# Performance work log

Measured on AMD Instinct MI355X. Metric: run time of the kernel, lower is better.

## Reference

```python
import jax, jax.numpy as jnp
import numpy as np

B, Q, S, D, H = 8, 100, 4096, 256, 8
HD = D // H
EPS = 1e-5


def layer_norm(x, g, b):
    mu = jnp.mean(x, axis=-1, keepdims=True)
    var = jnp.mean(jnp.square(x - mu), axis=-1, keepdims=True)
    return (x - mu) * jax.lax.rsqrt(var + EPS) * g + b


def mha(q_in, k_in, v_in, w_in, b_in, w_out, b_out, bias=None):
    # torch nn.MultiheadAttention math (batch_first, dropout=0)
    wq, wk, wv = jnp.split(w_in, 3, axis=0)
    bq, bk, bv = jnp.split(b_in, 3, axis=0)
    Bq, Lq, _ = q_in.shape
    Lk = k_in.shape[1]
    q = (q_in @ wq.T + bq).reshape(Bq, Lq, H, HD)
    k = (k_in @ wk.T + bk).reshape(Bq, Lk, H, HD)
    v = (v_in @ wv.T + bv).reshape(Bq, Lk, H, HD)
    scores = jnp.einsum('bqhd,bkhd->bhqk', q, k) / jnp.sqrt(jnp.asarray(HD, q.dtype))
    if bias is not None:
        scores = scores + bias  # [B,1,Q,S] broadcast over heads (same per head)
    attn = jax.nn.softmax(scores, axis=-1)
    out = jnp.einsum('bhqk,bkhd->bqhd', attn, v).reshape(Bq, Lq, D)
    return out @ w_out.T + b_out


def setup_inputs() -> dict:
    key = jax.random.key(0)
    ks = jax.random.split(key, 12)
    s = 0.02
    return {
        'queries': jax.random.normal(ks[0], (B, Q, D), jnp.float32),
        'pixel_feat': jax.random.normal(ks[1], (B, S, D), jnp.float32),
        'prev_mask': jax.random.normal(ks[2], (B, Q, S), jnp.float32),
        'cross_in_w': jax.random.normal(ks[3], (3 * D, D), jnp.float32) * s,
        'cross_in_b': jnp.zeros((3 * D,), jnp.float32),
        'cross_out_w': jax.random.normal(ks[4], (D, D), jnp.float32) * s,
        'cross_out_b': jnp.zeros((D,), jnp.float32),
        'self_in_w': jax.random.normal(ks[5], (3 * D, D), jnp.float32) * s,
        'self_in_b': jnp.zeros((3 * D,), jnp.float32),
        'self_out_w': jax.random.normal(ks[6], (D, D), jnp.float32) * s,
        'self_out_b': jnp.zeros((D,), jnp.float32),
        'ln_cross_g': jnp.ones((D,), jnp.float32),
        'ln_cross_b': jnp.zeros((D,), jnp.float32),
        'ln_self_g': jnp.ones((D,), jnp.float32),
        'ln_self_b': jnp.zeros((D,), jnp.float32),
        'ln_ffn_g': jnp.ones((D,), jnp.float32),
        'ln_ffn_b': jnp.zeros((D,), jnp.float32),
        'ffn_w1': jax.random.normal(ks[7], (4 * D, D), jnp.float32) * s,
        'ffn_b1': jnp.zeros((4 * D,), jnp.float32),
        'ffn_w2': jax.random.normal(ks[8], (D, 4 * D), jnp.float32) * s,
        'ffn_b2': jnp.zeros((D,), jnp.float32),
    }


def reference(queries, pixel_feat, prev_mask,
              cross_in_w, cross_in_b, cross_out_w, cross_out_b,
              self_in_w, self_in_b, self_out_w, self_out_b,
              ln_cross_g, ln_cross_b, ln_self_g, ln_self_b, ln_ffn_g, ln_ffn_b,
              ffn_w1, ffn_b1, ffn_w2, ffn_b2):
    # masked cross-attn bias (no-grad region in torch; boolean ops have no grad)
    region = jax.nn.sigmoid(prev_mask) > 0.5                    # [B,Q,S]
    any_pos = jnp.any(region, axis=-1, keepdims=True)
    region = jnp.where(any_pos, region, jnp.ones_like(region))
    bias = (~region).astype(queries.dtype) * -10000.0
    bias = bias[:, None, :, :]                                  # [B,1,Q,S]

    q_out = mha(layer_norm(queries, ln_cross_g, ln_cross_b), pixel_feat, pixel_feat,
                cross_in_w, cross_in_b, cross_out_w, cross_out_b, bias)
    queries = queries + q_out

    q_norm = layer_norm(queries, ln_self_g, ln_self_b)
    q_out = mha(q_norm, q_norm, q_norm, self_in_w, self_in_b, self_out_w, self_out_b)
    queries = queries + q_out

    h = layer_norm(queries, ln_ffn_g, ln_ffn_b)
    h = jax.nn.gelu(h @ ffn_w1.T + ffn_b1, approximate=False) @ ffn_w2.T + ffn_b2
    return queries + h
```

## Files before the change

kernel.cpp:

```cpp
#include <hip/hip_runtime.h>
#include <hip/hip_bf16.h>
#include <math.h>

#define BQ 100
#define SB 8
#define SS 4096
#define DD 256
#define HH 8
#define HDD 32
#define NSPLIT 4
#define SCHUNK (SS / NSPLIT)
#define MROWS 800

typedef __attribute__((ext_vector_type(8))) short bf16x8;
typedef __attribute__((ext_vector_type(4))) float f32x4;

__device__ inline unsigned short f2bf(float f) {
    union { float f; unsigned u; } v; v.f = f;
    unsigned r = v.u + 0x7fff + ((v.u >> 16) & 1);
    return (unsigned short)(r >> 16);
}

__device__ inline unsigned pkbf(float x, float y) {
    union { __hip_bfloat162 h; unsigned u; } c;
    c.h = __float22bfloat162_rn(make_float2(x, y));
    return c.u;
}

__device__ inline bf16x8 load_bf8(const float* p) {
    float4 a = *(const float4*)p;
    float4 b = *(const float4*)(p + 4);
    union { unsigned u[4]; bf16x8 v; } r;
    r.u[0] = pkbf(a.x, a.y); r.u[1] = pkbf(a.z, a.w);
    r.u[2] = pkbf(b.x, b.y); r.u[3] = pkbf(b.z, b.w);
    return r.v;
}

#define TM 128
#define TN 128
#define TK 32
#define LSTR 40

__global__ __launch_bounds__(256, 4) void stage1(
        const float* __restrict__ queries,
        const float* __restrict__ ln_g, const float* __restrict__ ln_b,
        const float* __restrict__ cw, const float* __restrict__ cb,
        float* __restrict__ q_cross,
        const float* __restrict__ pixel_feat,
        unsigned short* __restrict__ Kb, unsigned short* __restrict__ Vb,
        const float* __restrict__ mask, unsigned* __restrict__ Mbits) {
    __shared__ __align__(16) char smem[21504];
    const int bid = blockIdx.x;
    const int t = threadIdx.x;

    if (bid < 1024) {
        typedef unsigned short (*tile_t)[LSTR];
        tile_t As = (tile_t)smem;
        tile_t Bs = (tile_t)(smem + 128 * LSTR * 2);
        const float* A = pixel_feat;
        const float* W = cw + (size_t)DD * DD;
        const float* bias = cb + DD;
        int xcd = bid & 7, idx = bid >> 3;
        int mt = xcd + 8 * (idx >> 2);
        int nt = idx & 3;
        int m0 = mt * TM, n0 = nt * TN;
        int wave = t / 64, lane = t % 64;
        int wm = (wave % 2) * 64, wn = (wave / 2) * 64;
        int lr = t / 4, lc = (t % 4) * 8;
        int fr = lane % 16, quad = lane / 16;
        f32x4 acc[4][4] = {};
        for (int k0 = 0; k0 < DD; k0 += TK) {
            __syncthreads();
#pragma unroll
            for (int half = 0; half < 2; half++) {
                int r = lr + half * 64;
                float4 a0 = *(const float4*)(A + (size_t)(m0 + r) * DD + k0 + lc);
                float4 a1 = *(const float4*)(A + (size_t)(m0 + r) * DD + k0 + lc + 4);
                uint4 pa;
                pa.x = pkbf(a0.x, a0.y); pa.y = pkbf(a0.z, a0.w);
                pa.z = pkbf(a1.x, a1.y); pa.w = pkbf(a1.z, a1.w);
                *(uint4*)&As[r][lc] = pa;
                float4 b0 = *(const float4*)(W + (size_t)(n0 + r) * DD + k0 + lc);
                float4 b1 = *(const float4*)(W + (size_t)(n0 + r) * DD + k0 + lc + 4);
                uint4 pb;
                pb.x = pkbf(b0.x, b0.y); pb.y = pkbf(b0.z, b0.w);
                pb.z = pkbf(b1.x, b1.y); pb.w = pkbf(b1.z, b1.w);
                *(uint4*)&Bs[r][lc] = pb;
            }
            __syncthreads();
            bf16x8 af[4], bf[4];
#pragma unroll
            for (int mi = 0; mi < 4; mi++)
                af[mi] = *(const bf16x8*)&As[wm + mi * 16 + fr][quad * 8];
#pragma unroll
            for (int ni = 0; ni < 4; ni++)
                bf[ni] = *(const bf16x8*)&Bs[wn + ni * 16 + fr][quad * 8];
#pragma unroll
            for (int mi = 0; mi < 4; mi++)
#pragma unroll
                for (int ni = 0; ni < 4; ni++)
                    acc[mi][ni] = __builtin_amdgcn_mfma_f32_16x16x32_bf16(
                        af[mi], bf[ni], acc[mi][ni], 0, 0, 0);
        }
#pragma unroll
        for (int ni = 0; ni < 4; ni++) {
            int n = n0 + wn + ni * 16 + fr;
            float bv = bias[n];
            unsigned short* dst = (n < 256) ? Kb : Vb;
            int hh = (n >> 5) & 7, d = n & 31;
#pragma unroll
            for (int mi = 0; mi < 4; mi++) {
#pragma unroll
                for (int r = 0; r < 4; r++) {
                    int m = m0 + wm + mi * 16 + quad * 4 + r;
                    int bb = m >> 12, s = m & (SS - 1);
                    dst[((((size_t)bb * HH + hh) * SS + s) << 5) + d] =
                        f2bf(acc[mi][ni][r] + bv);
                }
            }
        }
    } else if (bid < 1824) {
        int row = bid - 1024;
        unsigned* words = (unsigned*)smem;
        unsigned* orred = (unsigned*)(smem + 512);
        int w = t >> 6, lane = t & 63;
        unsigned lor = 0;
        for (int i = 0; i < 16; i++) {
            int s = (w * 16 + i) * 64 + lane;
            unsigned long long bal = __ballot(mask[(size_t)row * SS + s] > 0.f);
            if (lane == 0) {
                words[(w * 16 + i) * 2] = (unsigned)bal;
                words[(w * 16 + i) * 2 + 1] = (unsigned)(bal >> 32);
            }
            lor |= (unsigned)(bal | (bal >> 32));
        }
        if (lane == 0) orred[w] = lor;
        __syncthreads();
        unsigned anyv = orred[0] | orred[1] | orred[2] | orred[3];
        if (t < 128) Mbits[(size_t)row * 128 + t] = anyv ? words[t] : 0xFFFFFFFFu;
    } else {
        typedef unsigned short (*arow_t)[264];
        arow_t Aq = (arow_t)smem;
        float* mu_s = (float*)(smem + 16896);
        float* rs_s = mu_s + 32;
        float (*prt)[8][2] = (float(*)[8][2])(rs_s + 32);
        int idx = bid - 1824;
        int nq = idx & 1, my = idx >> 1;
        int m0 = my * 32;
        int row = t & 31, cs = t >> 5;
        const float* xp = queries + (size_t)(m0 + row) * DD + cs * 32;
        float s = 0.f, ss = 0.f;
#pragma unroll
        for (int c = 0; c < 32; c += 4) {
            float4 v = *(const float4*)(xp + c);
            s += v.x + v.y + v.z + v.w;
            ss += v.x * v.x + v.y * v.y + v.z * v.z + v.w * v.w;
        }
        prt[row][cs][0] = s; prt[row][cs][1] = ss;
        __syncthreads();
        if (t < 32) {
            float sum = 0.f, sq = 0.f;
#pragma unroll
            for (int k = 0; k < 8; k++) { sum += prt[t][k][0]; sq += prt[t][k][1]; }
            float mu = sum * (1.0f / DD);
            float var = sq * (1.0f / DD) - mu * mu;
            mu_s[t] = mu;
            rs_s[t] = rsqrtf(var + 1e-5f);
        }
        __syncthreads();
        {
            float mu = mu_s[row], r = rs_s[row];
            int col0 = cs * 32;
#pragma unroll
            for (int c = 0; c < 32; c += 8) {
                int col = col0 + c;
                float4 v0 = *(const float4*)(xp + c);
                float4 v1 = *(const float4*)(xp + c + 4);
                float4 g0 = *(const float4*)(ln_g + col);
                float4 g1 = *(const float4*)(ln_g + col + 4);
                float4 b0 = *(const float4*)(ln_b + col);
                float4 b1 = *(const float4*)(ln_b + col + 4);
                uint4 pk;
                pk.x = pkbf((v0.x - mu) * r * g0.x + b0.x, (v0.y - mu) * r * g0.y + b0.y);
                pk.y = pkbf((v0.z - mu) * r * g0.z + b0.z, (v0.w - mu) * r * g0.w + b0.w);
                pk.z = pkbf((v1.x - mu) * r * g1.x + b1.x, (v1.y - mu) * r * g1.y + b1.y);
                pk.w = pkbf((v1.z - mu) * r * g1.z + b1.z, (v1.w - mu) * r * g1.w + b1.w);
                *(uint4*)&Aq[row][col] = pk;
            }
        }
        __syncthreads();
        int w = t >> 6, lane = t & 63;
        int fr = lane & 15, quad = lane >> 4;
        int n0 = nq * 128 + w * 32;
        f32x4 acc[2][2] = {};
        const float* Wp0 = cw + (size_t)(n0 + fr) * DD + quad * 8;
        const float* Wp1 = Wp0 + (size_t)16 * DD;
#pragma unroll
        for (int k0 = 0; k0 < DD; k0 += 32) {
            bf16x8 a0 = *(const bf16x8*)&Aq[fr][k0 + quad * 8];
            bf16x8 a1 = *(const bf16x8*)&Aq[16 + fr][k0 + quad * 8];
            bf16x8 w0 = load_bf8(Wp0 + k0);
            bf16x8 w1 = load_bf8(Wp1 + k0);
            acc[0][0] = __builtin_amdgcn_mfma_f32_16x16x32_bf16(a0, w0, acc[0][0], 0, 0, 0);
            acc[0][1] = __builtin_amdgcn_mfma_f32_16x16x32_bf16(a0, w1, acc[0][1], 0, 0, 0);
            acc[1][0] = __builtin_amdgcn_mfma_f32_16x16x32_bf16(a1, w0, acc[1][0], 0, 0, 0);
            acc[1][1] = __builtin_amdgcn_mfma_f32_16x16x32_bf16(a1, w1, acc[1][1], 0, 0, 0);
        }
#pragma unroll
        for (int ni = 0; ni < 2; ni++) {
            int n = n0 + ni * 16 + fr;
            float bv = cb[n];
#pragma unroll
            for (int mi = 0; mi < 2; mi++) {
#pragma unroll
                for (int r = 0; r < 4; r++) {
                    int m = m0 + mi * 16 + quad * 4 + r;
                    q_cross[(size_t)m * DD + n] = acc[mi][ni][r] + bv;
                }
            }
        }
    }
}

template<int MODE>
__global__ __launch_bounds__(64, 4) void ln_gemm(
        const float* __restrict__ X, const float* __restrict__ gam,
        const float* __restrict__ bet,
        const float* __restrict__ W, const float* __restrict__ bias,
        const float* __restrict__ res,
        float* __restrict__ C, int N) {
    __shared__ unsigned short As[32][264];
    __shared__ float mu_s[32], rs_s[32];
    __shared__ float prt[32][2][2];
    const int t = threadIdx.x;
    const int fr = t & 15, quad = t >> 4;
    const int m0 = blockIdx.y * 32, n0 = blockIdx.x * 32;
    const int row = t & 31, half = t >> 5;

    const float* xp = X + (size_t)(m0 + row) * DD + half * 128;
    float s = 0.f, ss = 0.f;
#pragma unroll
    for (int c = 0; c < 128; c += 4) {
        float4 v = *(const float4*)(xp + c);
        s += v.x + v.y + v.z + v.w;
        ss += v.x * v.x + v.y * v.y + v.z * v.z + v.w * v.w;
    }
    prt[row][half][0] = s;
    prt[row][half][1] = ss;
    __syncthreads();
    if (t < 32) {
        float sum = prt[t][0][0] + prt[t][1][0];
        float sq  = prt[t][0][1] + prt[t][1][1];
        float mu = sum * (1.0f / DD);
        float var = sq * (1.0f / DD) - mu * mu;
        mu_s[t] = mu;
        rs_s[t] = rsqrtf(var + 1e-5f);
    }
    __syncthreads();
    {
        float mu = mu_s[row], r = rs_s[row];
#pragma unroll
        for (int c = 0; c < 128; c += 8) {
            int col = half * 128 + c;
            float4 v0 = *(const float4*)(xp + c);
            float4 v1 = *(const float4*)(xp + c + 4);
            float4 g0 = *(const float4*)(gam + col);
            float4 g1 = *(const float4*)(gam + col + 4);
            float4 b0 = *(const float4*)(bet + col);
            float4 b1 = *(const float4*)(bet + col + 4);
            uint4 pk;
            pk.x = pkbf((v0.x - mu) * r * g0.x + b0.x, (v0.y - mu) * r * g0.y + b0.y);
            pk.y = pkbf((v0.z - mu) * r * g0.z + b0.z, (v0.w - mu) * r * g0.w + b0.w);
            pk.z = pkbf((v1.x - mu) * r * g1.x + b1.x, (v1.y - mu) * r * g1.y + b1.y);
            pk.w = pkbf((v1.z - mu) * r * g1.z + b1.z, (v1.w - mu) * r * g1.w + b1.w);
            *(uint4*)&As[row][col] = pk;
        }
    }
    __syncthreads();

    f32x4 acc[2][2] = {};
    const float* Wp0 = W + (size_t)(n0 + fr) * DD + quad * 8;
    const float* Wp1 = Wp0 + (size_t)16 * DD;
#pragma unroll
    for (int k0 = 0; k0 < DD; k0 += 32) {
        bf16x8 a0 = *(const bf16x8*)&As[fr][k0 + quad * 8];
        bf16x8 a1 = *(const bf16x8*)&As[16 + fr][k0 + quad * 8];
        bf16x8 w0 = load_bf8(Wp0 + k0);
        bf16x8 w1 = load_bf8(Wp1 + k0);
        acc[0][0] = __builtin_amdgcn_mfma_f32_16x16x32_bf16(a0, w0, acc[0][0], 0, 0, 0);
        acc[0][1] = __builtin_amdgcn_mfma_f32_16x16x32_bf16(a0, w1, acc[0][1], 0, 0, 0);
        acc[1][0] = __builtin_amdgcn_mfma_f32_16x16x32_bf16(a1, w0, acc[1][0], 0, 0, 0);
        acc[1][1] = __builtin_amdgcn_mfma_f32_16x16x32_bf16(a1, w1, acc[1][1], 0, 0, 0);
    }

#pragma unroll
    for (int ni = 0; ni < 2; ni++) {
        int n = n0 + ni * 16 + fr;
        float bv = bias[n];
#pragma unroll
        for (int mi = 0; mi < 2; mi++) {
#pragma unroll
            for (int r = 0; r < 4; r++) {
                int m = m0 + mi * 16 + quad * 4 + r;
                float v = acc[mi][ni][r] + bv;
                if (MODE == 1) {
                    v = 0.5f * v * (1.0f + erff(v * 0.70710678118654752f));
                } else if (MODE == 2) {
                    v += res[(size_t)m * N + n];
                }
                C[(size_t)m * N + n] = v;
            }
        }
    }
}

__global__ __launch_bounds__(64, 4) void comb_gemm(
        const float* __restrict__ Opart, const float* __restrict__ mpart,
        const float* __restrict__ lpart,
        const float* __restrict__ W, const float* __restrict__ bias,
        const float* __restrict__ res,
        float* __restrict__ C) {
    __shared__ unsigned short As[32][264];
    const int t = threadIdx.x;
    const int fr = t & 15, quad = t >> 4;
    const int m0 = blockIdx.y * 32, n0 = blockIdx.x * 32;
    const int row = t & 31, half = t >> 5;

    {
        int m = m0 + row;
        int b = m / BQ, q = m % BQ;
#pragma unroll
        for (int h = half * 4; h < half * 4 + 4; h++) {
            float mv[NSPLIT], wsp[NSPLIT];
            float mstar = -1e30f;
#pragma unroll
            for (int sp = 0; sp < NSPLIT; sp++) {
                mv[sp] = mpart[((size_t)(b * NSPLIT + sp) * HH + h) * BQ + q];
                mstar = fmaxf(mstar, mv[sp]);
            }
            float lstar = 0.f;
#pragma unroll
            for (int sp = 0; sp < NSPLIT; sp++) {
                wsp[sp] = __expf(mv[sp] - mstar);
                lstar += lpart[((size_t)(b * NSPLIT + sp) * HH + h) * BQ + q] * wsp[sp];
            }
            float inv = 1.0f / lstar;
#pragma unroll
            for (int d = 0; d < HDD; d += 8) {
                float o[8] = {};
#pragma unroll
                for (int sp = 0; sp < NSPLIT; sp++) {
                    const float* op = Opart +
                        ((size_t)(b * NSPLIT + sp) * BQ + q) * DD + h * HDD + d;
                    float4 a = *(const float4*)op;
                    float4 b4 = *(const float4*)(op + 4);
                    o[0] += a.x * wsp[sp];  o[1] += a.y * wsp[sp];
                    o[2] += a.z * wsp[sp];  o[3] += a.w * wsp[sp];
                    o[4] += b4.x * wsp[sp]; o[5] += b4.y * wsp[sp];
                    o[6] += b4.z * wsp[sp]; o[7] += b4.w * wsp[sp];
                }
                uint4 pk;
                pk.x = pkbf(o[0] * inv, o[1] * inv);
                pk.y = pkbf(o[2] * inv, o[3] * inv);
                pk.z = pkbf(o[4] * inv, o[5] * inv);
                pk.w = pkbf(o[6] * inv, o[7] * inv);
                *(uint4*)&As[row][h * HDD + d] = pk;
            }
        }
    }
    __syncthreads();

    f32x4 acc[2][2] = {};
    const float* Wp0 = W + (size_t)(n0 + fr) * DD + quad * 8;
    const float* Wp1 = Wp0 + (size_t)16 * DD;
#pragma unroll
    for (int k0 = 0; k0 < DD; k0 += 32) {
        bf16x8 a0 = *(const bf16x8*)&As[fr][k0 + quad * 8];
        bf16x8 a1 = *(const bf16x8*)&As[16 + fr][k0 + quad * 8];
        bf16x8 w0 = load_bf8(Wp0 + k0);
        bf16x8 w1 = load_bf8(Wp1 + k0);
        acc[0][0] = __builtin_amdgcn_mfma_f32_16x16x32_bf16(a0, w0, acc[0][0], 0, 0, 0);
        acc[0][1] = __builtin_amdgcn_mfma_f32_16x16x32_bf16(a0, w1, acc[0][1], 0, 0, 0);
        acc[1][0] = __builtin_amdgcn_mfma_f32_16x16x32_bf16(a1, w0, acc[1][0], 0, 0, 0);
        acc[1][1] = __builtin_amdgcn_mfma_f32_16x16x32_bf16(a1, w1, acc[1][1], 0, 0, 0);
    }

#pragma unroll
    for (int ni = 0; ni < 2; ni++) {
        int n = n0 + ni * 16 + fr;
        float bv = bias[n];
#pragma unroll
        for (int mi = 0; mi < 2; mi++) {
#pragma unroll
            for (int r = 0; r < 4; r++) {
                int m = m0 + mi * 16 + quad * 4 + r;
                float v = acc[mi][ni][r] + bv + res[(size_t)m * DD + n];
                C[(size_t)m * DD + n] = v;
            }
        }
    }
}

template<int KK, int SPLITK, int MODE>
__global__ __launch_bounds__(64, 4) void gemm_skinny2(
        const float* __restrict__ A, const float* __restrict__ W,
        const float* __restrict__ bias, const float* __restrict__ res,
        float* __restrict__ C, float* __restrict__ Cp, int N) {
    const int lane = threadIdx.x;
    const int fr = lane & 15, quad = lane >> 4;
    const int m0 = blockIdx.y * 32;
    const int n0 = blockIdx.x * 32;
    const int sk = blockIdx.z;
    const int KCH = KK / SPLITK;

    f32x4 acc[2][2] = {};
    const float* Ap0 = A + (size_t)(m0 + fr) * KK + sk * KCH + quad * 8;
    const float* Ap1 = Ap0 + (size_t)16 * KK;
    const float* Wp0 = W + (size_t)(n0 + fr) * KK + sk * KCH + quad * 8;
    const float* Wp1 = Wp0 + (size_t)16 * KK;

#pragma unroll
    for (int k0 = 0; k0 < KCH; k0 += 32) {
        bf16x8 a0 = load_bf8(Ap0 + k0);
        bf16x8 a1 = load_bf8(Ap1 + k0);
        bf16x8 w0 = load_bf8(Wp0 + k0);
        bf16x8 w1 = load_bf8(Wp1 + k0);
        acc[0][0] = __builtin_amdgcn_mfma_f32_16x16x32_bf16(a0, w0, acc[0][0], 0, 0, 0);
        acc[0][1] = __builtin_amdgcn_mfma_f32_16x16x32_bf16(a0, w1, acc[0][1], 0, 0, 0);
        acc[1][0] = __builtin_amdgcn_mfma_f32_16x16x32_bf16(a1, w0, acc[1][0], 0, 0, 0);
        acc[1][1] = __builtin_amdgcn_mfma_f32_16x16x32_bf16(a1, w1, acc[1][1], 0, 0, 0);
    }

    if (SPLITK == 1) {
#pragma unroll
        for (int ni = 0; ni < 2; ni++) {
            int n = n0 + ni * 16 + fr;
            float bv = bias[n];
#pragma unroll
            for (int mi = 0; mi < 2; mi++) {
#pragma unroll
                for (int r = 0; r < 4; r++) {
                    int m = m0 + mi * 16 + quad * 4 + r;
                    float v = acc[mi][ni][r] + bv;
                    if (MODE == 1) {
                        v = 0.5f * v * (1.0f + erff(v * 0.70710678118654752f));
                    } else if (MODE == 2) {
                        v += res[(size_t)m * N + n];
                    }
                    C[(size_t)m * N + n] = v;
                }
            }
        }
    } else {
        float* dst = Cp + (size_t)sk * MROWS * N;
#pragma unroll
        for (int ni = 0; ni < 2; ni++) {
            int n = n0 + ni * 16 + fr;
#pragma unroll
            for (int mi = 0; mi < 2; mi++) {
#pragma unroll
                for (int r = 0; r < 4; r++) {
                    int m = m0 + mi * 16 + quad * 4 + r;
                    dst[(size_t)m * N + n] = acc[mi][ni][r];
                }
            }
        }
    }
}

template<int SPLITK, int MODE>
__global__ void gemm_combine(const float* __restrict__ Cp,
                             const float* __restrict__ bias,
                             const float* __restrict__ res,
                             float* __restrict__ C, int N) {
    int m = blockIdx.x;
    for (int n = threadIdx.x; n < N; n += 256) {
        float v = bias[n];
#pragma unroll
        for (int sk = 0; sk < SPLITK; sk++)
            v += Cp[((size_t)sk * MROWS + m) * N + n];
        if (MODE == 1) {
            v = 0.5f * v * (1.0f + erff(v * 0.70710678118654752f));
        } else if (MODE == 2) {
            v += res[(size_t)m * N + n];
        }
        C[(size_t)m * N + n] = v;
    }
}

#define QT 64
#define ST 128

__global__ __launch_bounds__(256) void cross_attn_mfma(
        const float* __restrict__ Qm,
        const unsigned short* __restrict__ Kb,
        const unsigned short* __restrict__ Vb,
        const unsigned* __restrict__ Mbits,
        float* __restrict__ Opart,
        float* __restrict__ mpart,
        float* __restrict__ lpart) {
    __shared__ unsigned short Qs[QT][40];
    __shared__ unsigned short Ks[ST][40];
    __shared__ unsigned short Vt[HDD][136];
    __shared__ unsigned short Ps[QT][136];
    __shared__ unsigned Mq[QT][4];
    __shared__ float red[QT][17];
    __shared__ float m_s[QT], alpha_s[QT], l_s[QT];

    const int qb = blockIdx.x, h = blockIdx.y;
    const int b = blockIdx.z / NSPLIT, sp = blockIdx.z % NSPLIT;
    const int t = threadIdx.x;
    const int w = t >> 6, lane = t & 63;
    const int fr = lane & 15, quad = lane >> 4;
    const int q0 = qb * QT;
    const int qlim = min(BQ - q0, QT);

    {
        int q = t >> 2, c0 = (t & 3) * 8;
        float4 v0 = make_float4(0.f, 0.f, 0.f, 0.f), v1 = v0;
        if (q < qlim) {
            const float* qp = Qm + (size_t)(b * BQ + q0 + q) * DD + h * HDD + c0;
            v0 = *(const float4*)qp;
            v1 = *(const float4*)(qp + 4);
        }
        const float sc = 0.17677669529663687f;
        uint4 pq;
        pq.x = pkbf(v0.x * sc, v0.y * sc);
        pq.y = pkbf(v0.z * sc, v0.w * sc);
        pq.z = pkbf(v1.x * sc, v1.y * sc);
        pq.w = pkbf(v1.z * sc, v1.w * sc);
        *(uint4*)&Qs[q][c0] = pq;
        if (t < QT) { m_s[t] = -1e30f; l_s[t] = 0.f; }
    }

    f32x4 oacc[2] = {};
    const unsigned short* Kbase = Kb + (((size_t)(b * HH + h)) * SS << 5);
    const unsigned short* Vbase = Vb + (((size_t)(b * HH + h)) * SS << 5);

    for (int s0 = sp * SCHUNK; s0 < (sp + 1) * SCHUNK; s0 += ST) {
        __syncthreads();
        {
            int r = t >> 1, half = t & 1;
            const unsigned short* kp = Kbase + ((size_t)(s0 + r) << 5) + half * 16;
            *(uint4*)&Ks[r][half * 16] = *(const uint4*)kp;
            *(uint4*)&Ks[r][half * 16 + 8] = *(const uint4*)(kp + 8);
            const unsigned short* vp = Vbase + ((size_t)(s0 + r) << 5) + half * 16;
            union { uint4 u; unsigned short s[8]; } v0, v1;
            v0.u = *(const uint4*)vp;
            v1.u = *(const uint4*)(vp + 8);
#pragma unroll
            for (int j = 0; j < 8; j++) Vt[half * 16 + j][r] = v0.s[j];
#pragma unroll
            for (int j = 0; j < 8; j++) Vt[half * 16 + 8 + j][r] = v1.s[j];
        }
        {
            int q = t >> 2, wd = t & 3;
            unsigned mword = 0xFFFFFFFFu;
            if (q < qlim)
                mword = Mbits[(size_t)(b * BQ + q0 + q) * 128 + (s0 >> 5) + wd];
            Mq[q][wd] = mword;
        }
        __syncthreads();

        bf16x8 af[2];
#pragma unroll
        for (int mt = 0; mt < 2; mt++)
            af[mt] = *(const bf16x8*)&Ks[w * 32 + mt * 16 + fr][quad * 8];
        f32x4 st[2][4];
#pragma unroll
        for (int nt = 0; nt < 4; nt++) {
            bf16x8 bq = *(const bf16x8*)&Qs[nt * 16 + fr][quad * 8];
#pragma unroll
            for (int mt = 0; mt < 2; mt++) {
                f32x4 z = {0.f, 0.f, 0.f, 0.f};
                st[mt][nt] = __builtin_amdgcn_mfma_f32_16x16x32_bf16(af[mt], bq, z, 0, 0, 0);
            }
        }

        float pmax[4] = {-1e30f, -1e30f, -1e30f, -1e30f};
#pragma unroll
        for (int nt = 0; nt < 4; nt++) {
            unsigned mword = Mq[nt * 16 + fr][w];
#pragma unroll
            for (int mt = 0; mt < 2; mt++)
#pragma unroll
                for (int r = 0; r < 4; r++) {
                    int bitpos = mt * 16 + quad * 4 + r;
                    float v = st[mt][nt][r];
                    if (!((mword >> bitpos) & 1u)) v -= 10000.f;
                    st[mt][nt][r] = v;
                    pmax[nt] = fmaxf(pmax[nt], v);
                }
        }
#pragma unroll
        for (int nt = 0; nt < 4; nt++)
            red[nt * 16 + fr][w * 4 + quad] = pmax[nt];
        __syncthreads();

        if (t < QT) {
            float mt_ = -1e30f;
#pragma unroll
            for (int k = 0; k < 16; k++) mt_ = fmaxf(mt_, red[t][k]);
            float mo = m_s[t], mn = fmaxf(mo, mt_);
            m_s[t] = mn;
            alpha_s[t] = __expf(mo - mn);
        }
        __syncthreads();

        float psum[4] = {0.f, 0.f, 0.f, 0.f};
#pragma unroll
        for (int nt = 0; nt < 4; nt++) {
            float mrow = m_s[nt * 16 + fr];
#pragma unroll
            for (int mt = 0; mt < 2; mt++) {
                float p0 = __expf(st[mt][nt][0] - mrow);
                float p1 = __expf(st[mt][nt][1] - mrow);
                float p2 = __expf(st[mt][nt][2] - mrow);
                float p3 = __expf(st[mt][nt][3] - mrow);
                psum[nt] += p0 + p1 + p2 + p3;
                uint2 pk;
                pk.x = pkbf(p0, p1);
                pk.y = pkbf(p2, p3);
                *(uint2*)&Ps[nt * 16 + fr][w * 32 + mt * 16 + quad * 4] = pk;
            }
        }
#pragma unroll
        for (int nt = 0; nt < 4; nt++)
            red[nt * 16 + fr][w * 4 + quad] = psum[nt];
        __syncthreads();

        if (t < QT) {
            float s = 0.f;
#pragma unroll
            for (int k = 0; k < 16; k++) s += red[t][k];
            l_s[t] = l_s[t] * alpha_s[t] + s;
        }

#pragma unroll
        for (int r = 0; r < 4; r++) {
            float a = alpha_s[w * 16 + quad * 4 + r];
            oacc[0][r] *= a; oacc[1][r] *= a;
        }
#pragma unroll
        for (int k0 = 0; k0 < ST; k0 += 32) {
            bf16x8 ap = *(const bf16x8*)&Ps[w * 16 + fr][k0 + quad * 8];
            bf16x8 bv0 = *(const bf16x8*)&Vt[fr][k0 + quad * 8];
            bf16x8 bv1 = *(const bf16x8*)&Vt[16 + fr][k0 + quad * 8];
            oacc[0] = __builtin_amdgcn_mfma_f32_16x16x32_bf16(ap, bv0, oacc[0], 0, 0, 0);
            oacc[1] = __builtin_amdgcn_mfma_f32_16x16x32_bf16(ap, bv1, oacc[1], 0, 0, 0);
        }
    }
    __syncthreads();

    int part = b * NSPLIT + sp;
    if (t < qlim) {
        mpart[((size_t)part * HH + h) * BQ + q0 + t] = m_s[t];
        lpart[((size_t)part * HH + h) * BQ + q0 + t] = l_s[t];
    }
#pragma unroll
    for (int nd = 0; nd < 2; nd++) {
#pragma unroll
        for (int r = 0; r < 4; r++) {
            int q = w * 16 + quad * 4 + r;
            if (q < qlim)
                Opart[((size_t)part * BQ + q0 + q) * DD + h * HDD + nd * 16 + fr] = oacc[nd][r];
        }
    }
}

__global__ void attn_kernel(const float* __restrict__ Qm, int sq, int qo0,
                            const float* __restrict__ Km, int sk, int ko0,
                            const float* __restrict__ Vm, int sv, int vo0,
                            float* __restrict__ Out, int so, int oo0,
                            int Slen, int Qlen, float scale) {
    int q = blockIdx.x, h = blockIdx.y, b = blockIdx.z;
    int tid = threadIdx.x;
    __shared__ float qv[32];
    __shared__ float sc[128];
    __shared__ float red[256];
    __shared__ float part[8][33];
    int qrow = b * Qlen + q;
    if (tid < 32) qv[tid] = Qm[(size_t)qrow * sq + qo0 + h * HDD + tid] * scale;
    __syncthreads();

    float lmax = -1e30f;
    for (int s = tid; s < Slen; s += 256) {
        const float* kp = Km + (size_t)(b * Slen + s) * sk + ko0 + h * HDD;
        float dot = 0.f;
#pragma unroll
        for (int d = 0; d < HDD; d += 4) {
            float4 k4 = *(const float4*)(kp + d);
            dot += qv[d] * k4.x + qv[d + 1] * k4.y + qv[d + 2] * k4.z + qv[d + 3] * k4.w;
        }
        sc[s] = dot;
        lmax = fmaxf(lmax, dot);
    }
    red[tid] = lmax; __syncthreads();
    for (int off = 128; off > 0; off >>= 1) {
        if (tid < off) red[tid] = fmaxf(red[tid], red[tid + off]);
        __syncthreads();
    }
    float m = red[0];
    __syncthreads();
    float lsum = 0.f;
    for (int s = tid; s < Slen; s += 256) {
        float e = __expf(sc[s] - m);
        sc[s] = e;
        lsum += e;
    }
    red[tid] = lsum; __syncthreads();
    for (int off = 128; off > 0; off >>= 1) {
        if (tid < off) red[tid] += red[tid + off];
        __syncthreads();
    }
    float inv = 1.0f / red[0];

    int d = tid & 31, g = tid >> 5;
    float acc = 0.f;
    for (int s = g; s < Slen; s += 8)
        acc += sc[s] * Vm[(size_t)(b * Slen + s) * sv + vo0 + h * HDD + d];
    part[g][d] = acc; __syncthreads();
    if (g == 0) {
        float t = 0.f;
#pragma unroll
        for (int gg = 0; gg < 8; gg++) t += part[gg][d];
        Out[(size_t)qrow * so + oo0 + h * HDD + d] = t * inv;
    }
}

extern "C" void kernel_launch(void* const* d_in, const int* in_sizes, int n_in,
                              void* d_out, int out_size, void* d_ws, size_t ws_size,
                              hipStream_t stream) {
    const float* queries    = (const float*)d_in[0];
    const float* pixel_feat = (const float*)d_in[1];
    const float* prev_mask  = (const float*)d_in[2];
    const float* cross_in_w  = (const float*)d_in[3];
    const float* cross_in_b  = (const float*)d_in[4];
    const float* cross_out_w = (const float*)d_in[5];
    const float* cross_out_b = (const float*)d_in[6];
    const float* self_in_w   = (const float*)d_in[7];
    const float* self_in_b   = (const float*)d_in[8];
    const float* self_out_w  = (const float*)d_in[9];
    const float* self_out_b  = (const float*)d_in[10];
    const float* ln_cross_g  = (const float*)d_in[11];
    const float* ln_cross_b  = (const float*)d_in[12];
    const float* ln_self_g   = (const float*)d_in[13];
    const float* ln_self_b   = (const float*)d_in[14];
    const float* ln_ffn_g    = (const float*)d_in[15];
    const float* ln_ffn_b    = (const float*)d_in[16];
    const float* ffn_w1 = (const float*)d_in[17];
    const float* ffn_b1 = (const float*)d_in[18];
    const float* ffn_w2 = (const float*)d_in[19];
    const float* ffn_b2 = (const float*)d_in[20];
    float* out = (float*)d_out;

    const int NQ = SB * BQ;
    const int NK = SB * SS;

    float* ws = (float*)d_ws;
    unsigned* Mbits = (unsigned*)ws;   ws += (size_t)NQ * 128;
    float* q_cross  = ws;              ws += (size_t)NQ * DD;
    unsigned short* Kbk = (unsigned short*)ws;
    ws += (size_t)NK * DD / 2;
    unsigned short* Vbk = (unsigned short*)ws;
    ws += (size_t)NK * DD / 2;
    float* queries1 = ws;              ws += (size_t)NQ * DD;
    float* qkv      = ws;              ws += (size_t)NQ * 3 * DD;
    float* attn2    = ws;              ws += (size_t)NQ * DD;
    float* queries2 = ws;              ws += (size_t)NQ * DD;
    float* ffn_h    = ws;              ws += (size_t)NQ * 4 * DD;
    float* Csplit   = ws;              ws += (size_t)4 * MROWS * DD;
    float* Opart    = ws;              ws += (size_t)SB * NSPLIT * BQ * DD;
    float* mpart    = ws;              ws += (size_t)SB * NSPLIT * HH * BQ;
    float* lpart    = ws;              ws += (size_t)SB * NSPLIT * HH * BQ;

    const float scale = 0.17677669529663687f;

    stage1<<<1874, 256, 0, stream>>>(
        queries, ln_cross_g, ln_cross_b, cross_in_w, cross_in_b, q_cross,
        pixel_feat, Kbk, Vbk, prev_mask, Mbits);

    cross_attn_mfma<<<dim3(2, HH, SB * NSPLIT), 256, 0, stream>>>(
        q_cross, Kbk, Vbk, Mbits, Opart, mpart, lpart);
    comb_gemm<<<dim3(8, 25), 64, 0, stream>>>(
        Opart, mpart, lpart, cross_out_w, cross_out_b, queries, queries1);

    ln_gemm<0><<<dim3(24, 25), 64, 0, stream>>>(
        queries1, ln_self_g, ln_self_b, self_in_w, self_in_b, nullptr,
        qkv, 3 * DD);
    attn_kernel<<<dim3(BQ, HH, SB), 256, 0, stream>>>(
        qkv, 3 * DD, 0, qkv, 3 * DD, DD, qkv, 3 * DD, 2 * DD,
        attn2, DD, 0, BQ, BQ, scale);
    gemm_skinny2<256, 1, 2><<<dim3(8, 25), 64, 0, stream>>>(
        attn2, self_out_w, self_out_b, queries1, queries2, nullptr, DD);

    ln_gemm<1><<<dim3(32, 25), 64, 0, stream>>>(
        queries2, ln_ffn_g, ln_ffn_b, ffn_w1, ffn_b1, nullptr,
        ffn_h, 4 * DD);
    gemm_skinny2<1024, 4, 2><<<dim3(8, 25, 4), 64, 0, stream>>>(
        ffn_h, ffn_w2, ffn_b2, nullptr, nullptr, Csplit, DD);
    gemm_combine<4, 2><<<MROWS, 256, 0, stream>>>(
        Csplit, ffn_b2, queries2, out, DD);
}
```

Measured before the change: 258.8 us.

## Pre-convert all weights to bf16 once and load them directly in GEMMs

Adds a wprep kernel that converts every weight matrix to bf16 into a workspace buffer once per call, and all GEMMs then read bf16 weights directly instead of loading fp32 and packing per tile. The K/V projection in stage1 drops its shared-memory B tile, reads weight fragments straight from global memory into registers, and prefetches the next A tile into registers while the current one is being consumed. The mask bit-packing loads all 16 values before balloting. This trades one extra launch and weight traffic for less conversion work and halved weight bandwidth in the main GEMMs.

```diff
diff --git a/kernel.cpp b/kernel.cpp
--- a/kernel.cpp
+++ b/kernel.cpp
@@ -41,10 +41,42 @@
 #define TK 32
 #define LSTR 40
 
+#define WOFF_CW   0
+#define WOFF_SIW  196608
+#define WOFF_COW  393216
+#define WOFF_SOW  458752
+#define WOFF_F1   524288
+#define WOFF_F2   786432
+#define WTOT      1048576
+
+__global__ __launch_bounds__(256) void wprep(
+        const float* __restrict__ cw, const float* __restrict__ siw,
+        const float* __restrict__ cow, const float* __restrict__ sow,
+        const float* __restrict__ f1, const float* __restrict__ f2,
+        unsigned short* __restrict__ o) {
+    int b = blockIdx.x;
+    const float* src; size_t so, doff;
+    if (b < 96)       { src = cw;  so = (size_t)b * 2048;         doff = WOFF_CW; }
+    else if (b < 192) { src = siw; so = (size_t)(b - 96) * 2048;  doff = WOFF_SIW; }
+    else if (b < 224) { src = cow; so = (size_t)(b - 192) * 2048; doff = WOFF_COW; }
+    else if (b < 256) { src = sow; so = (size_t)(b - 224) * 2048; doff = WOFF_SOW; }
+    else if (b < 384) { src = f1;  so = (size_t)(b - 256) * 2048; doff = WOFF_F1; }
+    else              { src = f2;  so = (size_t)(b - 384) * 2048; doff = WOFF_F2; }
+    int t = threadIdx.x;
+    const float* p = src + so + (size_t)t * 8;
+    float4 a = *(const float4*)p;
+    float4 c = *(const float4*)(p + 4);
+    uint4 pk;
+    pk.x = pkbf(a.x, a.y); pk.y = pkbf(a.z, a.w);
+    pk.z = pkbf(c.x, c.y); pk.w = pkbf(c.z, c.w);
+    *(uint4*)(o + doff + so + (size_t)t * 8) = pk;
+}
+
 __global__ __launch_bounds__(256, 4) void stage1(
         const float* __restrict__ queries,
         const float* __restrict__ ln_g, const float* __restrict__ ln_b,
-        const float* __restrict__ cw, const float* __restrict__ cb,
+        const unsigned short* __restrict__ wbf,
+        const float* __restrict__ cb,
         float* __restrict__ q_cross,
         const float* __restrict__ pixel_feat,
         unsigned short* __restrict__ Kb, unsigned short* __restrict__ Vb,
@@ -56,51 +88,59 @@
     if (bid < 1024) {
         typedef unsigned short (*tile_t)[LSTR];
         tile_t As = (tile_t)smem;
-        tile_t Bs = (tile_t)(smem + 128 * LSTR * 2);
         const float* A = pixel_feat;
-        const float* W = cw + (size_t)DD * DD;
+        const unsigned short* Wb = wbf + (size_t)DD * DD;
         const float* bias = cb + DD;
         int xcd = bid & 7, idx = bid >> 3;
         int mt = xcd + 8 * (idx >> 2);
-        int nt = idx & 3;
-        int m0 = mt * TM, n0 = nt * TN;
+        int ntl = idx & 3;
+        int m0 = mt * TM, n0 = ntl * TN;
         int wave = t / 64, lane = t % 64;
         int wm = (wave % 2) * 64, wn = (wave / 2) * 64;
         int lr = t / 4, lc = (t % 4) * 8;
         int fr = lane % 16, quad = lane / 16;
         f32x4 acc[4][4] = {};
+
+        const float* Arow0 = A + (size_t)(m0 + lr) * DD + lc;
+        const float* Arow1 = A + (size_t)(m0 + lr + 64) * DD + lc;
+        const unsigned short* Wfr = Wb + (size_t)(n0 + wn + fr) * DD + quad * 8;
+
+        float4 p00 = *(const float4*)(Arow0);
+        float4 p01 = *(const float4*)(Arow0 + 4);
+        float4 p10 = *(const float4*)(Arow1);
+        float4 p11 = *(const float4*)(Arow1 + 4);
+
         for (int k0 = 0; k0 < DD; k0 += TK) {
             __syncthreads();
-#pragma unroll
-            for (int half = 0; half < 2; half++) {
-                int r = lr + half * 64;
-                float4 a0 = *(const float4*)(A + (size_t)(m0 + r) * DD + k0 + lc);
-                float4 a1 = *(const float4*)(A + (size_t)(m0 + r) * DD + k0 + lc + 4);
-                uint4 pa;
-                pa.x = pkbf(a0.x, a0.y); pa.y = pkbf(a0.z, a0.w);
-                pa.z = pkbf(a1.x, a1.y); pa.w = pkbf(a1.z, a1.w);
-                *(uint4*)&As[r][lc] = pa;
-                float4 b0 = *(const float4*)(W + (size_t)(n0 + r) * DD + k0 + lc);
-                float4 b1 = *(const float4*)(W + (size_t)(n0 + r) * DD + k0 + lc + 4);
-                uint4 pb;
-                pb.x = pkbf(b0.x, b0.y); pb.y = pkbf(b0.z, b0.w);
-                pb.z = pkbf(b1.x, b1.y); pb.w = pkbf(b1.z, b1.w);
-                *(uint4*)&Bs[r][lc] = pb;
-            }
+            uint4 pk0, pk1;
+            pk0.x = pkbf(p00.x, p00.y); pk0.y = pkbf(p00.z, p00.w);
+            pk0.z = pkbf(p01.x, p01.y); pk0.w = pkbf(p01.z, p01.w);
+            *(uint4*)&As[lr][lc] = pk0;
+            pk1.x = pkbf(p10.x, p10.y); pk1.y = pkbf(p10.z, p10.w);
+            pk1.z = pkbf(p11.x, p11.y); pk1.w = pkbf(p11.z, p11.w);
+            *(uint4*)&As[lr + 64][lc] = pk1;
+            if (k0 < DD - TK) {
+                p00 = *(const float4*)(Arow0 + k0 + 32);
+                p01 = *(const float4*)(Arow0 + k0 + 36);
+                p10 = *(const float4*)(Arow1 + k0 + 32);
+                p11 = *(const float4*)(Arow1 + k0 + 36);
+            }
+            bf16x8 bv0 = *(const bf16x8*)(Wfr + k0);
+            bf16x8 bv1 = *(const bf16x8*)(Wfr + (size_t)16 * DD + k0);
+            bf16x8 bv2 = *(const bf16x8*)(Wfr + (size_t)32 * DD + k0);
+            bf16x8 bv3 = *(const bf16x8*)(Wfr + (size_t)48 * DD + k0);
             __syncthreads();
-            bf16x8 af[4], bf[4];
+            bf16x8 af[4];
 #pragma unroll
             for (int mi = 0; mi < 4; mi++)
                 af[mi] = *(const bf16x8*)&As[wm + mi * 16 + fr][quad * 8];
 #pragma unroll
-            for (int ni = 0; ni < 4; ni++)
-                bf[ni] = *(const bf16x8*)&Bs[wn + ni * 16 + fr][quad * 8];
-#pragma unroll
-            for (int mi = 0; mi < 4; mi++)
-#pragma unroll
-                for (int ni = 0; ni < 4; ni++)
-                    acc[mi][ni] = __builtin_amdgcn_mfma_f32_16x16x32_bf16(
-                        af[mi], bf[ni], acc[mi][ni], 0, 0, 0);
+            for (int mi = 0; mi < 4; mi++) {
+                acc[mi][0] = __builtin_amdgcn_mfma_f32_16x16x32_bf16(af[mi], bv0, acc[mi][0], 0, 0, 0);
+                acc[mi][1] = __builtin_amdgcn_mfma_f32_16x16x32_bf16(af[mi], bv1, acc[mi][1], 0, 0, 0);
+                acc[mi][2] = __builtin_amdgcn_mfma_f32_16x16x32_bf16(af[mi], bv2, acc[mi][2], 0, 0, 0);
+                acc[mi][3] = __builtin_amdgcn_mfma_f32_16x16x32_bf16(af[mi], bv3, acc[mi][3], 0, 0, 0);
+            }
         }
 #pragma unroll
         for (int ni = 0; ni < 4; ni++) {
@@ -124,10 +164,14 @@
         unsigned* words = (unsigned*)smem;
         unsigned* orred = (unsigned*)(smem + 512);
         int w = t >> 6, lane = t & 63;
+        const float* mp = mask + (size_t)row * SS + lane;
+        float mv[16];
+#pragma unroll
+        for (int i = 0; i < 16; i++) mv[i] = mp[(w * 16 + i) * 64];
         unsigned lor = 0;
+#pragma unroll
         for (int i = 0; i < 16; i++) {
-            int s = (w * 16 + i) * 64 + lane;
-            unsigned long long bal = __ballot(mask[(size_t)row * SS + s] > 0.f);
+            unsigned long long bal = __ballot(mv[i] > 0.f);
             if (lane == 0) {
                 words[(w * 16 + i) * 2] = (unsigned)bal;
                 words[(w * 16 + i) * 2 + 1] = (unsigned)(bal >> 32);
@@ -193,14 +237,14 @@
         int fr = lane & 15, quad = lane >> 4;
         int n0 = nq * 128 + w * 32;
         f32x4 acc[2][2] = {};
-        const float* Wp0 = cw + (size_t)(n0 + fr) * DD + quad * 8;
-        const float* Wp1 = Wp0 + (size_t)16 * DD;
+        const unsigned short* Wq0 = wbf + (size_t)(n0 + fr) * DD + quad * 8;
+        const unsigned short* Wq1 = Wq0 + (size_t)16 * DD;
 #pragma unroll
         for (int k0 = 0; k0 < DD; k0 += 32) {
             bf16x8 a0 = *(const bf16x8*)&Aq[fr][k0 + quad * 8];
             bf16x8 a1 = *(const bf16x8*)&Aq[16 + fr][k0 + quad * 8];
-            bf16x8 w0 = load_bf8(Wp0 + k0);
-            bf16x8 w1 = load_bf8(Wp1 + k0);
+            bf16x8 w0 = *(const bf16x8*)(Wq0 + k0);
+            bf16x8 w1 = *(const bf16x8*)(Wq1 + k0);
             acc[0][0] = __builtin_amdgcn_mfma_f32_16x16x32_bf16(a0, w0, acc[0][0], 0, 0, 0);
             acc[0][1] = __builtin_amdgcn_mfma_f32_16x16x32_bf16(a0, w1, acc[0][1], 0, 0, 0);
             acc[1][0] = __builtin_amdgcn_mfma_f32_16x16x32_bf16(a1, w0, acc[1][0], 0, 0, 0);
@@ -226,7 +270,7 @@
 __global__ __launch_bounds__(64, 4) void ln_gemm(
         const float* __restrict__ X, const float* __restrict__ gam,
         const float* __restrict__ bet,
-        const float* __restrict__ W, const float* __restrict__ bias,
+        const unsigned short* __restrict__ W, const float* __restrict__ bias,
         const float* __restrict__ res,
         float* __restrict__ C, int N) {
     __shared__ unsigned short As[32][264];
@@ -279,14 +323,14 @@
     __syncthreads();
 
     f32x4 acc[2][2] = {};
-    const float* Wp0 = W + (size_t)(n0 + fr) * DD + quad * 8;
-    const float* Wp1 = Wp0 + (size_t)16 * DD;
+    const unsigned short* Wp0 = W + (size_t)(n0 + fr) * DD + quad * 8;
+    const unsigned short* Wp1 = Wp0 + (size_t)16 * DD;
 #pragma unroll
     for (int k0 = 0; k0 < DD; k0 += 32) {
         bf16x8 a0 = *(const bf16x8*)&As[fr][k0 + quad * 8];
         bf16x8 a1 = *(const bf16x8*)&As[16 + fr][k0 + quad * 8];
-        bf16x8 w0 = load_bf8(Wp0 + k0);
-        bf16x8 w1 = load_bf8(Wp1 + k0);
+        bf16x8 w0 = *(const bf16x8*)(Wp0 + k0);
+        bf16x8 w1 = *(const bf16x8*)(Wp1 + k0);
         acc[0][0] = __builtin_amdgcn_mfma_f32_16x16x32_bf16(a0, w0, acc[0][0], 0, 0, 0);
         acc[0][1] = __builtin_amdgcn_mfma_f32_16x16x32_bf16(a0, w1, acc[0][1], 0, 0, 0);
         acc[1][0] = __builtin_amdgcn_mfma_f32_16x16x32_bf16(a1, w0, acc[1][0], 0, 0, 0);
@@ -317,7 +361,7 @@
 __global__ __launch_bounds__(64, 4) void comb_gemm(
         const float* __restrict__ Opart, const float* __restrict__ mpart,
         const float* __restrict__ lpart,
-        const float* __restrict__ W, const float* __restrict__ bias,
+        const unsigned short* __restrict__ W, const float* __restrict__ bias,
         const float* __restrict__ res,
         float* __restrict__ C) {
     __shared__ unsigned short As[32][264];
@@ -371,14 +415,14 @@
     __syncthreads();
 
     f32x4 acc[2][2] = {};
-    const float* Wp0 = W + (size_t)(n0 + fr) * DD + quad * 8;
-    const float* Wp1 = Wp0 + (size_t)16 * DD;
+    const unsigned short* Wp0 = W + (size_t)(n0 + fr) * DD + quad * 8;
+    const unsigned short* Wp1 = Wp0 + (size_t)16 * DD;
 #pragma unroll
     for (int k0 = 0; k0 < DD; k0 += 32) {
         bf16x8 a0 = *(const bf16x8*)&As[fr][k0 + quad * 8];
         bf16x8 a1 = *(const bf16x8*)&As[16 + fr][k0 + quad * 8];
-        bf16x8 w0 = load_bf8(Wp0 + k0);
-        bf16x8 w1 = load_bf8(Wp1 + k0);
+        bf16x8 w0 = *(const bf16x8*)(Wp0 + k0);
+        bf16x8 w1 = *(const bf16x8*)(Wp1 + k0);
         acc[0][0] = __builtin_amdgcn_mfma_f32_16x16x32_bf16(a0, w0, acc[0][0], 0, 0, 0);
         acc[0][1] = __builtin_amdgcn_mfma_f32_16x16x32_bf16(a0, w1, acc[0][1], 0, 0, 0);
         acc[1][0] = __builtin_amdgcn_mfma_f32_16x16x32_bf16(a1, w0, acc[1][0], 0, 0, 0);
@@ -403,7 +447,7 @@
 
 template<int KK, int SPLITK, int MODE>
 __global__ __launch_bounds__(64, 4) void gemm_skinny2(
-        const float* __restrict__ A, const float* __restrict__ W,
+        const float* __restrict__ A, const unsigned short* __restrict__ W,
         const float* __restrict__ bias, const float* __restrict__ res,
         float* __restrict__ C, float* __restrict__ Cp, int N) {
     const int lane = threadIdx.x;
@@ -416,15 +460,15 @@
     f32x4 acc[2][2] = {};
     const float* Ap0 = A + (size_t)(m0 + fr) * KK + sk * KCH + quad * 8;
     const float* Ap1 = Ap0 + (size_t)16 * KK;
-    const float* Wp0 = W + (size_t)(n0 + fr) * KK + sk * KCH + quad * 8;
-    const float* Wp1 = Wp0 + (size_t)16 * KK;
+    const unsigned short* Wp0 = W + (size_t)(n0 + fr) * KK + sk * KCH + quad * 8;
+    const unsigned short* Wp1 = Wp0 + (size_t)16 * KK;
 
 #pragma unroll
     for (int k0 = 0; k0 < KCH; k0 += 32) {
         bf16x8 a0 = load_bf8(Ap0 + k0);
         bf16x8 a1 = load_bf8(Ap1 + k0);
-        bf16x8 w0 = load_bf8(Wp0 + k0);
-        bf16x8 w1 = load_bf8(Wp1 + k0);
+        bf16x8 w0 = *(const bf16x8*)(Wp0 + k0);
+        bf16x8 w1 = *(const bf16x8*)(Wp1 + k0);
         acc[0][0] = __builtin_amdgcn_mfma_f32_16x16x32_bf16(a0, w0, acc[0][0], 0, 0, 0);
         acc[0][1] = __builtin_amdgcn_mfma_f32_16x16x32_bf16(a0, w1, acc[0][1], 0, 0, 0);
         acc[1][0] = __builtin_amdgcn_mfma_f32_16x16x32_bf16(a1, w0, acc[1][0], 0, 0, 0);
@@ -773,32 +817,36 @@
     float* Opart    = ws;              ws += (size_t)SB * NSPLIT * BQ * DD;
     float* mpart    = ws;              ws += (size_t)SB * NSPLIT * HH * BQ;
     float* lpart    = ws;              ws += (size_t)SB * NSPLIT * HH * BQ;
+    unsigned short* wbf = (unsigned short*)ws;
 
     const float scale = 0.17677669529663687f;
 
+    wprep<<<512, 256, 0, stream>>>(
+        cross_in_w, self_in_w, cross_out_w, self_out_w, ffn_w1, ffn_w2, wbf);
+
     stage1<<<1874, 256, 0, stream>>>(
-        queries, ln_cross_g, ln_cross_b, cross_in_w, cross_in_b, q_cross,
+        queries, ln_cross_g, ln_cross_b, wbf, cross_in_b, q_cross,
         pixel_feat, Kbk, Vbk, prev_mask, Mbits);
 
     cross_attn_mfma<<<dim3(2, HH, SB * NSPLIT), 256, 0, stream>>>(
         q_cross, Kbk, Vbk, Mbits, Opart, mpart, lpart);
     comb_gemm<<<dim3(8, 25), 64, 0, stream>>>(
-        Opart, mpart, lpart, cross_out_w, cross_out_b, queries, queries1);
+        Opart, mpart, lpart, wbf + WOFF_COW, cross_out_b, queries, queries1);
 
     ln_gemm<0><<<dim3(24, 25), 64, 0, stream>>>(
-        queries1, ln_self_g, ln_self_b, self_in_w, self_in_b, nullptr,
+        queries1, ln_self_g, ln_self_b, wbf + WOFF_SIW, self_in_b, nullptr,
         qkv, 3 * DD);
     attn_kernel<<<dim3(BQ, HH, SB), 256, 0, stream>>>(
         qkv, 3 * DD, 0, qkv, 3 * DD, DD, qkv, 3 * DD, 2 * DD,
         attn2, DD, 0, BQ, BQ, scale);
     gemm_skinny2<256, 1, 2><<<dim3(8, 25), 64, 0, stream>>>(
-        attn2, self_out_w, self_out_b, queries1, queries2, nullptr, DD);
+        attn2, wbf + WOFF_SOW, self_out_b, queries1, queries2, nullptr, DD);
 
     ln_gemm<1><<<dim3(32, 25), 64, 0, stream>>>(
-        queries2, ln_ffn_g, ln_ffn_b, ffn_w1, ffn_b1, nullptr,
+        queries2, ln_ffn_g, ln_ffn_b, wbf + WOFF_F1, ffn_b1, nullptr,
         ffn_h, 4 * DD);
     gemm_skinny2<1024, 4, 2><<<dim3(8, 25, 4), 64, 0, stream>>>(
-        ffn_h, ffn_w2, ffn_b2, nullptr, nullptr, Csplit, DD);
+        ffn_h, wbf + WOFF_F2, ffn_b2, nullptr, nullptr, Csplit, DD);
     gemm_combine<4, 2><<<MROWS, 256, 0, stream>>>(
         Csplit, ffn_b2, queries2, out, DD);
 }
```

Result: faster. 253.4 us (-2.1%).
